# Optimization experiments

Measured on AMD Instinct MI355X. Metric: run time of the kernel, lower is better.

Reference implementation:

```python
import jax, jax.numpy as jnp
import numpy as np

EMBED = 512
NH = 8
HD = EMBED // NH
NL = 12
FFN = 2048
TD = 16  # latent_channels * patch_size**2 = 4*4


def _ln(x, g, b):
    m = x.mean(-1, keepdims=True)
    v = ((x - m) ** 2).mean(-1, keepdims=True)
    return (x - m) * jax.lax.rsqrt(v + 1e-5) * g + b


def _pos_emb(H, W, d):
    # faithful to get_2d_rope_embedding: cosine 1D embeddings along h and w, concatenated
    dh = d // 2
    inv = 1.0 / (10000.0 ** (jnp.arange(dh, dtype=jnp.float32) / dh))
    peh = jnp.cos(jnp.arange(H, dtype=jnp.float32)[:, None] * inv[None, :])  # (H, dh)
    pew = jnp.cos(jnp.arange(W, dtype=jnp.float32)[:, None] * inv[None, :])  # (W, dh)
    pe = jnp.concatenate([
        jnp.broadcast_to(peh[:, None, :], (H, W, dh)),
        jnp.broadcast_to(pew[None, :, :], (H, W, dh)),
    ], axis=-1)
    return pe.reshape(H * W, d)


def setup_inputs() -> dict:
    key = jax.random.key(0)
    ks = jax.random.split(key, 20)
    B, L = 8, 1024
    s = 0.02
    inp = {
        'x': jax.random.normal(ks[0], (B, L, TD), jnp.float32),
        'token_mask': jnp.ones((B, L), jnp.int32),
        'W_in': s * jax.random.normal(ks[1], (TD, EMBED), jnp.float32),
        'b_in': jnp.zeros((EMBED,), jnp.float32),
        'ln1_g': jnp.ones((NL, EMBED), jnp.float32),
        'ln1_b': jnp.zeros((NL, EMBED), jnp.float32),
        'Wq': s * jax.random.normal(ks[2], (NL, EMBED, EMBED), jnp.float32),
        'Wk': s * jax.random.normal(ks[3], (NL, EMBED, EMBED), jnp.float32),
        'Wv': s * jax.random.normal(ks[4], (NL, EMBED, EMBED), jnp.float32),
        'Wo': s * jax.random.normal(ks[5], (NL, EMBED, EMBED), jnp.float32),
        'ln2_g': jnp.ones((NL, EMBED), jnp.float32),
        'ln2_b': jnp.zeros((NL, EMBED), jnp.float32),
        'W1': s * jax.random.normal(ks[6], (NL, EMBED, FFN), jnp.float32),
        'W2': s * jax.random.normal(ks[7], (NL, EMBED, FFN), jnp.float32),
        'W3': s * jax.random.normal(ks[8], (NL, FFN, EMBED), jnp.float32),
        'W_out': s * jax.random.normal(ks[9], (EMBED, TD), jnp.float32),
        'b_out': jnp.zeros((TD,), jnp.float32),
        'H': 32,
        'W': 32,
    }
    return inp


def reference(x, token_mask, W_in, b_in, ln1_g, ln1_b, Wq, Wk, Wv, Wo,
              ln2_g, ln2_b, W1, W2, W3, W_out, b_out, H, W):
    B, L, _ = x.shape
    scale = 1.0 / np.sqrt(HD).astype(np.float32)
    h = x @ W_in + b_in + _pos_emb(H, W, EMBED)[None]  # (B, L, E)
    # (B,1,1,L) additive mask, -1e9 at padded positions
    mask = (token_mask == 0)[:, None, None, :].astype(h.dtype) * (-1e9)

    def block(h, p):
        g1, b1, wq, wk, wv, wo, g2, b2, w1, w2, w3 = p
        xn = _ln(h, g1, b1)
        q = (xn @ wq).reshape(B, L, NH, HD)
        k = (xn @ wk).reshape(B, L, NH, HD)
        v = (xn @ wv).reshape(B, L, NH, HD)
        s = jnp.einsum('blhd,bmhd->bhlm', q, k) * scale + mask
        a = jax.nn.softmax(s, axis=-1)
        o = jnp.einsum('bhlm,bmhd->blhd', a, v).reshape(B, L, EMBED) @ wo
        h = h + o
        xn = _ln(h, g2, b2)
        h = h + (jax.nn.silu(xn @ w1) * (xn @ w2)) @ w3
        return h, None

    h, _ = jax.lax.scan(block, h, (ln1_g, ln1_b, Wq, Wk, Wv, Wo, ln2_g, ln2_b, W1, W2, W3))
    return h @ W_out + b_out  # (B, L, TD)
```

## Files before the change

kernel.cpp:

```cpp
#include <hip/hip_runtime.h>

typedef __attribute__((ext_vector_type(8))) short short8;
typedef __attribute__((ext_vector_type(4))) float f32x4;
typedef __attribute__((ext_vector_type(4))) unsigned short us4;

#define MFMA_BF16(a,b,c) __builtin_amdgcn_mfma_f32_16x16x32_bf16((a),(b),(c),0,0,0)

__device__ __forceinline__ unsigned short f2bf(float f) {
  unsigned int u = __float_as_uint(f);
  u += 0x7fffu + ((u >> 16) & 1u);
  return (unsigned short)(u >> 16);
}

__device__ __forceinline__ int xcd_swz(int lid, int nwg) {
  return (lid & 7) * (nwg >> 3) + (lid >> 3);
}

__global__ __launch_bounds__(256) void wtrans_kernel(const float* __restrict__ src,
                                                     unsigned short* __restrict__ dst,
                                                     int R, int C) {
  __shared__ float tile[32][33];
  int c0 = blockIdx.x * 32, r0 = blockIdx.y * 32;
  const float* s = src + (size_t)blockIdx.z * R * C;
  unsigned short* d = dst + (size_t)blockIdx.z * R * C;
  int tx = threadIdx.x, ty = threadIdx.y;
#pragma unroll
  for (int i = 0; i < 32; i += 8)
    tile[ty + i][tx] = s[(size_t)(r0 + ty + i) * C + c0 + tx];
  __syncthreads();
#pragma unroll
  for (int i = 0; i < 32; i += 8)
    d[(size_t)(c0 + ty + i) * R + r0 + tx] = f2bf(tile[tx][ty + i]);
}

__global__ __launch_bounds__(128) void embed_kernel(const float* __restrict__ x,
                                                    const float* __restrict__ Win,
                                                    const float* __restrict__ bin,
                                                    float* __restrict__ h) {
  __shared__ float xs[16];
  int m = blockIdx.x, t = threadIdx.x;
  if (t < 16) xs[t] = x[m * 16 + t];
  __syncthreads();
  int l = m & 1023, hi = l >> 5, wi = l & 31;
#pragma unroll
  for (int e0 = 0; e0 < 512; e0 += 128) {
    int e = e0 + t;
    float a = bin[e];
#pragma unroll
    for (int kk = 0; kk < 16; kk++) a += xs[kk] * Win[kk * 512 + e];
    int j = e & 255;
    float p = (e < 256) ? (float)hi : (float)wi;
    float inv = expf((float)j * (-9.210340371976184f / 256.0f));
    a += cosf(p * inv);
    h[(size_t)m * 512 + e] = a;
  }
}

__global__ __launch_bounds__(256) void ln_kernel(const float* __restrict__ h,
                                                 const float* __restrict__ gw,
                                                 const float* __restrict__ bw,
                                                 unsigned short* __restrict__ xn) {
  int row = blockIdx.x * 4 + (threadIdx.x >> 6);
  int lane = threadIdx.x & 63;
  const f32x4* hr = (const f32x4*)&h[(size_t)row * 512];
  f32x4 v0 = hr[lane], v1 = hr[lane + 64];
  float s = v0[0]+v0[1]+v0[2]+v0[3] + v1[0]+v1[1]+v1[2]+v1[3];
  float q = v0[0]*v0[0]+v0[1]*v0[1]+v0[2]*v0[2]+v0[3]*v0[3]
          + v1[0]*v1[0]+v1[1]*v1[1]+v1[2]*v1[2]+v1[3]*v1[3];
#pragma unroll
  for (int o = 1; o < 64; o <<= 1) { s += __shfl_xor(s, o); q += __shfl_xor(q, o); }
  float mean = s * (1.0f / 512.0f);
  float var = q * (1.0f / 512.0f) - mean * mean;
  float rstd = rsqrtf(var + 1e-5f);
  f32x4 g0 = ((const f32x4*)gw)[lane], g1 = ((const f32x4*)gw)[lane + 64];
  f32x4 b0 = ((const f32x4*)bw)[lane], b1 = ((const f32x4*)bw)[lane + 64];
  us4 w0, w1;
#pragma unroll
  for (int r = 0; r < 4; r++) {
    w0[r] = f2bf((v0[r] - mean) * rstd * g0[r] + b0[r]);
    w1[r] = f2bf((v1[r] - mean) * rstd * g1[r] + b1[r]);
  }
  *(us4*)&xn[(size_t)row * 512 + lane * 4] = w0;
  *(us4*)&xn[(size_t)row * 512 + 256 + lane * 4] = w1;
}

__global__ __launch_bounds__(256) void qkv_gemm(const unsigned short* __restrict__ xn,
                                                const unsigned short* __restrict__ wtq,
                                                const unsigned short* __restrict__ wtk,
                                                const unsigned short* __restrict__ wtv,
                                                unsigned short* __restrict__ qo,
                                                unsigned short* __restrict__ ko,
                                                unsigned short* __restrict__ vt) {
  __shared__ short8 As[1024];
  __shared__ short8 Bs[1024];
  int n0 = blockIdx.x * 128, m0 = blockIdx.y * 128;
  int sel = n0 >> 9;
  const short8* wt = (const short8*)(sel == 0 ? wtq : sel == 1 ? wtk : wtv);
  int nw = n0 & 511;
  const short8* A8 = (const short8*)xn;
  int tid = threadIdx.x, wid = tid >> 6, lane = tid & 63;
  int wr = wid >> 1, wc = wid & 1, c16 = lane & 15, g = lane >> 4;
  const short8* aSrc[4];
  const short8* bSrc[4];
#pragma unroll
  for (int s = 0; s < 4; s++) {
    int sub = wid * 4 + s, rg = sub >> 1, kc = sub & 1;
    aSrc[s] = A8 + (size_t)(m0 + rg * 16 + c16) * 64 + kc * 4 + g;
    bSrc[s] = wt + (size_t)(nw + rg * 16 + c16) * 64 + kc * 4 + g;
  }
  f32x4 acc[4][4] = {};
  short8 ra[4], rb[4];
#pragma unroll
  for (int s = 0; s < 4; s++) { ra[s] = aSrc[s][0]; rb[s] = bSrc[s][0]; }
  for (int kt = 0; kt < 8; kt++) {
    __syncthreads();
#pragma unroll
    for (int s = 0; s < 4; s++) {
      As[(wid * 4 + s) * 64 + lane] = ra[s];
      Bs[(wid * 4 + s) * 64 + lane] = rb[s];
    }
    if (kt < 7) {
#pragma unroll
      for (int s = 0; s < 4; s++) {
        ra[s] = aSrc[s][(kt + 1) * 8];
        rb[s] = bSrc[s][(kt + 1) * 8];
      }
    }
    __syncthreads();
#pragma unroll
    for (int kc = 0; kc < 2; kc++) {
      short8 af[4], bf[4];
#pragma unroll
      for (int mf = 0; mf < 4; mf++) af[mf] = As[((wr * 4 + mf) * 2 + kc) * 64 + lane];
#pragma unroll
      for (int nf = 0; nf < 4; nf++) bf[nf] = Bs[((wc * 4 + nf) * 2 + kc) * 64 + lane];
#pragma unroll
      for (int mf = 0; mf < 4; mf++)
#pragma unroll
        for (int nf = 0; nf < 4; nf++)
          acc[mf][nf] = MFMA_BF16(af[mf], bf[nf], acc[mf][nf]);
    }
  }
  if (sel < 2) {
    unsigned short* out = sel == 0 ? qo : ko;
#pragma unroll
    for (int mf = 0; mf < 4; mf++)
#pragma unroll
      for (int nf = 0; nf < 4; nf++) {
        int col = nw + wc * 64 + nf * 16 + c16;
#pragma unroll
        for (int r = 0; r < 4; r++) {
          int row = m0 + wr * 64 + mf * 16 + g * 4 + r;
          out[(size_t)row * 512 + col] = f2bf(acc[mf][nf][r]);
        }
      }
  } else {
    int b8 = (m0 >> 10) * 8;
    int loff = (m0 & 1023) + wr * 64;
#pragma unroll
    for (int mf = 0; mf < 4; mf++)
#pragma unroll
      for (int nf = 0; nf < 4; nf++) {
        int c = nw + wc * 64 + nf * 16 + c16;
        int bh = b8 + (c >> 6), d = c & 63;
        us4 w;
#pragma unroll
        for (int r = 0; r < 4; r++) w[r] = f2bf(acc[mf][nf][r]);
        *(us4*)&vt[(size_t)(bh * 64 + d) * 1024 + loff + mf * 16 + g * 4] = w;
      }
  }
}

__global__ __launch_bounds__(256) void gemm_res(const unsigned short* __restrict__ A,
                                                const unsigned short* __restrict__ Wt,
                                                float* __restrict__ h, int Kd8, int nkt64) {
  __shared__ short8 As[1024];
  __shared__ short8 Bs[1024];
  int n0 = blockIdx.x * 128, m0 = blockIdx.y * 128;
  const short8* A8 = (const short8*)A;
  const short8* W8 = (const short8*)Wt;
  int tid = threadIdx.x, wid = tid >> 6, lane = tid & 63;
  int wr = wid >> 1, wc = wid & 1, c16 = lane & 15, g = lane >> 4;
  const short8* aSrc[4];
  const short8* bSrc[4];
#pragma unroll
  for (int s = 0; s < 4; s++) {
    int sub = wid * 4 + s, rg = sub >> 1, kc = sub & 1;
    aSrc[s] = A8 + (size_t)(m0 + rg * 16 + c16) * Kd8 + kc * 4 + g;
    bSrc[s] = W8 + (size_t)(n0 + rg * 16 + c16) * Kd8 + kc * 4 + g;
  }
  f32x4 acc[4][4] = {};
  short8 ra[4], rb[4];
#pragma unroll
  for (int s = 0; s < 4; s++) { ra[s] = aSrc[s][0]; rb[s] = bSrc[s][0]; }
  for (int kt = 0; kt < nkt64; kt++) {
    __syncthreads();
#pragma unroll
    for (int s = 0; s < 4; s++) {
      As[(wid * 4 + s) * 64 + lane] = ra[s];
      Bs[(wid * 4 + s) * 64 + lane] = rb[s];
    }
    if (kt + 1 < nkt64) {
#pragma unroll
      for (int s = 0; s < 4; s++) {
        ra[s] = aSrc[s][(kt + 1) * 8];
        rb[s] = bSrc[s][(kt + 1) * 8];
      }
    }
    __syncthreads();
#pragma unroll
    for (int kc = 0; kc < 2; kc++) {
      short8 af[4], bf[4];
#pragma unroll
      for (int mf = 0; mf < 4; mf++) af[mf] = As[((wr * 4 + mf) * 2 + kc) * 64 + lane];
#pragma unroll
      for (int nf = 0; nf < 4; nf++) bf[nf] = Bs[((wc * 4 + nf) * 2 + kc) * 64 + lane];
#pragma unroll
      for (int mf = 0; mf < 4; mf++)
#pragma unroll
        for (int nf = 0; nf < 4; nf++)
          acc[mf][nf] = MFMA_BF16(af[mf], bf[nf], acc[mf][nf]);
    }
  }
#pragma unroll
  for (int mf = 0; mf < 4; mf++)
#pragma unroll
    for (int nf = 0; nf < 4; nf++) {
      int col = n0 + wc * 64 + nf * 16 + c16;
#pragma unroll
      for (int r = 0; r < 4; r++) {
        int row = m0 + wr * 64 + mf * 16 + g * 4 + r;
        h[(size_t)row * 512 + col] += acc[mf][nf][r];
      }
    }
}

__global__ __launch_bounds__(256) void ffn_gemm(const unsigned short* __restrict__ xn,
                                                const unsigned short* __restrict__ w1t,
                                                const unsigned short* __restrict__ w2t,
                                                unsigned short* __restrict__ gout) {
  __shared__ short8 As[1024];
  __shared__ short8 B1s[1024];
  __shared__ short8 B2s[1024];
  int n0 = blockIdx.x * 128, m0 = blockIdx.y * 128;
  const short8* A8 = (const short8*)xn;
  const short8* W18 = (const short8*)w1t;
  const short8* W28 = (const short8*)w2t;
  int tid = threadIdx.x, wid = tid >> 6, lane = tid & 63;
  int wr = wid >> 1, wc = wid & 1, c16 = lane & 15, g = lane >> 4;
  const short8* aSrc[4];
  const short8* b1Src[4];
  const short8* b2Src[4];
#pragma unroll
  for (int s = 0; s < 4; s++) {
    int sub = wid * 4 + s, rg = sub >> 1, kc = sub & 1;
    aSrc[s]  = A8  + (size_t)(m0 + rg * 16 + c16) * 64 + kc * 4 + g;
    b1Src[s] = W18 + (size_t)(n0 + rg * 16 + c16) * 64 + kc * 4 + g;
    b2Src[s] = W28 + (size_t)(n0 + rg * 16 + c16) * 64 + kc * 4 + g;
  }
  f32x4 acc1[4][4] = {};
  f32x4 acc2[4][4] = {};
  short8 ra[4], rb1[4], rb2[4];
#pragma unroll
  for (int s = 0; s < 4; s++) {
    ra[s] = aSrc[s][0]; rb1[s] = b1Src[s][0]; rb2[s] = b2Src[s][0];
  }
  for (int kt = 0; kt < 8; kt++) {
    __syncthreads();
#pragma unroll
    for (int s = 0; s < 4; s++) {
      As [(wid * 4 + s) * 64 + lane] = ra[s];
      B1s[(wid * 4 + s) * 64 + lane] = rb1[s];
      B2s[(wid * 4 + s) * 64 + lane] = rb2[s];
    }
    if (kt < 7) {
#pragma unroll
      for (int s = 0; s < 4; s++) {
        ra[s]  = aSrc[s][(kt + 1) * 8];
        rb1[s] = b1Src[s][(kt + 1) * 8];
        rb2[s] = b2Src[s][(kt + 1) * 8];
      }
    }
    __syncthreads();
#pragma unroll
    for (int kc = 0; kc < 2; kc++) {
      short8 af[4], b1f[4], b2f[4];
#pragma unroll
      for (int mf = 0; mf < 4; mf++) af[mf] = As[((wr * 4 + mf) * 2 + kc) * 64 + lane];
#pragma unroll
      for (int nf = 0; nf < 4; nf++) {
        b1f[nf] = B1s[((wc * 4 + nf) * 2 + kc) * 64 + lane];
        b2f[nf] = B2s[((wc * 4 + nf) * 2 + kc) * 64 + lane];
      }
#pragma unroll
      for (int mf = 0; mf < 4; mf++)
#pragma unroll
        for (int nf = 0; nf < 4; nf++) {
          acc1[mf][nf] = MFMA_BF16(af[mf], b1f[nf], acc1[mf][nf]);
          acc2[mf][nf] = MFMA_BF16(af[mf], b2f[nf], acc2[mf][nf]);
        }
    }
  }
#pragma unroll
  for (int mf = 0; mf < 4; mf++)
#pragma unroll
    for (int nf = 0; nf < 4; nf++) {
      int col = n0 + wc * 64 + nf * 16 + c16;
#pragma unroll
      for (int r = 0; r < 4; r++) {
        int row = m0 + wr * 64 + mf * 16 + g * 4 + r;
        float xx = acc1[mf][nf][r];
        float yy = acc2[mf][nf][r];
        float sg = xx / (1.0f + __expf(-xx));
        gout[(size_t)row * 2048 + col] = f2bf(sg * yy);
      }
    }
}

__global__ __launch_bounds__(256) void attn_kernel(const unsigned short* __restrict__ q,
                                                   const unsigned short* __restrict__ k,
                                                   const unsigned short* __restrict__ vt,
                                                   const int* __restrict__ tmsk,
                                                   unsigned short* __restrict__ o) {
  __shared__ short8 Ks[512];
  __shared__ short8 Vs[512];
  __shared__ uint2  Pb[2048];
  __shared__ f32x4  maskv[256];

  int s = xcd_swz((int)blockIdx.x, 512);
  int qb = s & 7;
  int bh = s >> 3;
  int b = bh >> 3, hh = bh & 7;
  int tid = threadIdx.x, wid = tid >> 6, lane = tid & 63;
  int c16 = lane & 15, gq = lane >> 4;
  int qrow0 = qb * 128 + wid * 32;

  const short8* q8 = (const short8*)q;
  const short8* k8 = (const short8*)k;
  const short8* v8 = (const short8*)vt;

  short8 qf[2][2];
#pragma unroll
  for (int nf = 0; nf < 2; nf++)
#pragma unroll
    for (int dc = 0; dc < 2; dc++)
      qf[nf][dc] = q8[(size_t)(b * 1024 + qrow0 + nf * 16 + c16) * 64 + hh * 8 + dc * 4 + gq];

  {
    int4 mm = ((const int4*)(tmsk + b * 1024))[tid];
    f32x4 ma;
    ma[0] = (mm.x == 0) ? -1e9f : 0.0f;
    ma[1] = (mm.y == 0) ? -1e9f : 0.0f;
    ma[2] = (mm.z == 0) ? -1e9f : 0.0f;
    ma[3] = (mm.w == 0) ? -1e9f : 0.0f;
    maskv[tid] = ma;
  }

  short8 rk[2], rv[2];
#pragma unroll
  for (int ss = 0; ss < 2; ss++) {
    int sub = wid * 2 + ss;
    rk[ss] = k8[(size_t)(b * 1024 + (sub >> 1) * 16 + c16) * 64 + hh * 8 + (sub & 1) * 4 + gq];
    rv[ss] = v8[(size_t)(bh * 64 + (sub >> 1) * 16 + c16) * 128 + (sub & 1) * 4 + gq];
  }

  float mrun[2] = {-1e30f, -1e30f};
  float lrun[2] = {0.0f, 0.0f};
  f32x4 accO[4][2] = {};

  for (int kt = 0; kt < 16; kt++) {
    __syncthreads();
#pragma unroll
    for (int ss = 0; ss < 2; ss++) {
      int sub = wid * 2 + ss;
      Ks[sub * 64 + lane] = rk[ss];
      Vs[sub * 64 + lane] = rv[ss];
    }
    if (kt < 15) {
      int kt2 = kt + 1;
#pragma unroll
      for (int ss = 0; ss < 2; ss++) {
        int sub = wid * 2 + ss;
        rk[ss] = k8[(size_t)(b * 1024 + kt2 * 64 + (sub >> 1) * 16 + c16) * 64 + hh * 8 + (sub & 1) * 4 + gq];
        rv[ss] = v8[(size_t)(bh * 64 + (sub >> 1) * 16 + c16) * 128 + kt2 * 8 + (sub & 1) * 4 + gq];
      }
    }
    __syncthreads();

    f32x4 sT[4][2] = {};
#pragma unroll
    for (int mf = 0; mf < 4; mf++) {
      short8 ka0 = Ks[(mf * 2 + 0) * 64 + lane];
      short8 ka1 = Ks[(mf * 2 + 1) * 64 + lane];
#pragma unroll
      for (int nf = 0; nf < 2; nf++) {
        sT[mf][nf] = MFMA_BF16(ka0, qf[nf][0], sT[mf][nf]);
        sT[mf][nf] = MFMA_BF16(ka1, qf[nf][1], sT[mf][nf]);
      }
    }

#pragma unroll
    for (int nf = 0; nf < 2; nf++) {
      float pv[4][4];
      float tm = -1e30f;
#pragma unroll
      for (int mf = 0; mf < 4; mf++) {
        f32x4 mk = maskv[kt * 16 + mf * 4 + gq];
#pragma unroll
        for (int r = 0; r < 4; r++) {
          float sv = sT[mf][nf][r] * 0.125f + mk[r];
          pv[mf][r] = sv;
          tm = fmaxf(tm, sv);
        }
      }
      tm = fmaxf(tm, __shfl_xor(tm, 16));
      tm = fmaxf(tm, __shfl_xor(tm, 32));
      float mn = fmaxf(mrun[nf], tm);
      float fac = __expf(mrun[nf] - mn);
      mrun[nf] = mn;
      float ts = 0.0f;
#pragma unroll
      for (int mf = 0; mf < 4; mf++)
#pragma unroll
        for (int r = 0; r < 4; r++) {
          float p = __expf(pv[mf][r] - mn);
          pv[mf][r] = p;
          ts += p;
        }
      ts += __shfl_xor(ts, 16);
      ts += __shfl_xor(ts, 32);
      lrun[nf] = lrun[nf] * fac + ts;
#pragma unroll
      for (int dmf = 0; dmf < 4; dmf++) accO[dmf][nf] *= fac;
#pragma unroll
      for (int mf = 0; mf < 4; mf++) {
        unsigned lo = (unsigned)f2bf(pv[mf][0]) | ((unsigned)f2bf(pv[mf][1]) << 16);
        unsigned hi = (unsigned)f2bf(pv[mf][2]) | ((unsigned)f2bf(pv[mf][3]) << 16);
        int kk = mf >> 1;
        int gr = (mf & 1) * 2 + (gq >> 1);
        uint2 t2; t2.x = lo; t2.y = hi;
        Pb[wid * 512 + ((nf * 2 + kk) * 64 + gr * 16 + c16) * 2 + (gq & 1)] = t2;
      }
    }
    __syncthreads();

    const short8* Pb8 = (const short8*)Pb;
#pragma unroll
    for (int nf = 0; nf < 2; nf++) {
      short8 pb0 = Pb8[wid * 256 + (nf * 2 + 0) * 64 + lane];
      short8 pb1 = Pb8[wid * 256 + (nf * 2 + 1) * 64 + lane];
#pragma unroll
      for (int dmf = 0; dmf < 4; dmf++) {
        short8 va0 = Vs[(dmf * 2 + 0) * 64 + lane];
        short8 va1 = Vs[(dmf * 2 + 1) * 64 + lane];
        accO[dmf][nf] = MFMA_BF16(va0, pb0, accO[dmf][nf]);
        accO[dmf][nf] = MFMA_BF16(va1, pb1, accO[dmf][nf]);
      }
    }
  }

#pragma unroll
  for (int nf = 0; nf < 2; nf++) {
    float inv = 1.0f / lrun[nf];
    int row = b * 1024 + qrow0 + nf * 16 + c16;
#pragma unroll
    for (int dmf = 0; dmf < 4; dmf++) {
      us4 w;
#pragma unroll
      for (int r = 0; r < 4; r++) w[r] = f2bf(accO[dmf][nf][r] * inv);
      *(us4*)&o[(size_t)row * 512 + hh * 64 + dmf * 16 + gq * 4] = w;
    }
  }
}

__global__ __launch_bounds__(128) void out_kernel(const float* __restrict__ h,
                                                  const float* __restrict__ Wout,
                                                  const float* __restrict__ bout,
                                                  float* __restrict__ out) {
  __shared__ f32x4 hs4[8][128];
  __shared__ f32x4 Ws4[16][129];
  int t = threadIdx.x;
  int rb = blockIdx.x * 8;
  float* hsf = (float*)hs4;
  float* wsf = (float*)Ws4;
  for (int i = t; i < 4096; i += 128) hsf[i] = h[(size_t)rb * 512 + i];
  for (int i = t; i < 8192; i += 128) wsf[(i & 15) * 516 + (i >> 4)] = Wout[i];
  __syncthreads();
  int r = t >> 4, c = t & 15;
  float acc = bout[c];
  for (int k4 = 0; k4 < 128; k4++) {
    f32x4 a = hs4[r][k4];
    f32x4 w = Ws4[c][k4];
    acc += a[0]*w[0] + a[1]*w[1] + a[2]*w[2] + a[3]*w[3];
  }
  out[(rb + r) * 16 + c] = acc;
}

extern "C" void kernel_launch(void* const* d_in, const int* in_sizes, int n_in,
                              void* d_out, int out_size, void* d_ws, size_t ws_size,
                              hipStream_t stream) {
  const float* x    = (const float*)d_in[0];
  const int*   tmsk = (const int*)d_in[1];
  const float* Win  = (const float*)d_in[2];
  const float* bin  = (const float*)d_in[3];
  const float* ln1g = (const float*)d_in[4];
  const float* ln1b = (const float*)d_in[5];
  const float* Wq   = (const float*)d_in[6];
  const float* Wk   = (const float*)d_in[7];
  const float* Wv   = (const float*)d_in[8];
  const float* Wo   = (const float*)d_in[9];
  const float* ln2g = (const float*)d_in[10];
  const float* ln2b = (const float*)d_in[11];
  const float* W1   = (const float*)d_in[12];
  const float* W2   = (const float*)d_in[13];
  const float* W3   = (const float*)d_in[14];
  const float* Wout = (const float*)d_in[15];
  const float* bout = (const float*)d_in[16];
  float* outp = (float*)d_out;

  char* ws = (char*)d_ws;
  unsigned short* wtq = (unsigned short*)(ws + 0);
  unsigned short* wtk = (unsigned short*)(ws + 6291456);
  unsigned short* wtv = (unsigned short*)(ws + 12582912);
  unsigned short* wto = (unsigned short*)(ws + 18874368);
  unsigned short* wt1 = (unsigned short*)(ws + 25165824);
  unsigned short* wt2 = (unsigned short*)(ws + 50331648);
  unsigned short* wt3 = (unsigned short*)(ws + 75497472);
  float*          h   = (float*)(ws + 100663296);
  unsigned short* xn  = (unsigned short*)(ws + 117440512);
  unsigned short* qb  = (unsigned short*)(ws + 125829120);
  unsigned short* kb  = (unsigned short*)(ws + 134217728);
  unsigned short* vtb = (unsigned short*)(ws + 150994944);
  unsigned short* ob  = (unsigned short*)(ws + 159383552);
  unsigned short* gb  = (unsigned short*)(ws + 167772160);

  dim3 tb(32, 8);
  wtrans_kernel<<<dim3(16, 16, 12), tb, 0, stream>>>(Wq, wtq, 512, 512);
  wtrans_kernel<<<dim3(16, 16, 12), tb, 0, stream>>>(Wk, wtk, 512, 512);
  wtrans_kernel<<<dim3(16, 16, 12), tb, 0, stream>>>(Wv, wtv, 512, 512);
  wtrans_kernel<<<dim3(16, 16, 12), tb, 0, stream>>>(Wo, wto, 512, 512);
  wtrans_kernel<<<dim3(64, 16, 12), tb, 0, stream>>>(W1, wt1, 512, 2048);
  wtrans_kernel<<<dim3(64, 16, 12), tb, 0, stream>>>(W2, wt2, 512, 2048);
  wtrans_kernel<<<dim3(16, 64, 12), tb, 0, stream>>>(W3, wt3, 2048, 512);

  embed_kernel<<<8192, 128, 0, stream>>>(x, Win, bin, h);

  for (int l = 0; l < 12; l++) {
    ln_kernel<<<2048, 256, 0, stream>>>(h, ln1g + l * 512, ln1b + l * 512, xn);
    qkv_gemm<<<dim3(12, 64), 256, 0, stream>>>(xn,
        wtq + (size_t)l * 262144, wtk + (size_t)l * 262144, wtv + (size_t)l * 262144,
        qb, kb, vtb);
    attn_kernel<<<512, 256, 0, stream>>>(qb, kb, vtb, tmsk, ob);
    gemm_res<<<dim3(4, 64), 256, 0, stream>>>(ob, wto + (size_t)l * 262144, h, 64, 8);
    ln_kernel<<<2048, 256, 0, stream>>>(h, ln2g + l * 512, ln2b + l * 512, xn);
    ffn_gemm<<<dim3(16, 64), 256, 0, stream>>>(xn,
        wt1 + (size_t)l * 1048576, wt2 + (size_t)l * 1048576, gb);
    gemm_res<<<dim3(4, 64), 256, 0, stream>>>(gb, wt3 + (size_t)l * 1048576, h, 256, 32);
  }
  out_kernel<<<1024, 128, 0, stream>>>(h, Wout, bout, outp);

  (void)in_sizes; (void)n_in; (void)out_size; (void)ws_size;
}
```

Baseline: 2.519 ms.

## Enlarge QKV/FFN GEMM tiles to 256 rows and add lazy softmax rescaling

The QKV and FFN GEMMs now use 512-thread blocks covering 256 rows by 128 columns, so each weight tile loaded into shared memory is reused by twice as many rows and the grid shrinks by half. The attention softmax moves to base-2 exponentials with the log2(e) factor folded into the score scale and mask. It also skips rescaling the running max and accumulators unless some lane's max grows by more than 8. The goal is less weight traffic and fewer exp and rescale operations, at the cost of more LDS per block, possibly lower occupancy, and a looser running-max bound in the softmax.

```diff
diff --git a/kernel.cpp b/kernel.cpp
--- a/kernel.cpp
+++ b/kernel.cpp
@@ -84,16 +84,16 @@
   *(us4*)&xn[(size_t)row * 512 + 256 + lane * 4] = w1;
 }
 
-__global__ __launch_bounds__(256) void qkv_gemm(const unsigned short* __restrict__ xn,
+__global__ __launch_bounds__(512) void qkv_gemm(const unsigned short* __restrict__ xn,
                                                 const unsigned short* __restrict__ wtq,
                                                 const unsigned short* __restrict__ wtk,
                                                 const unsigned short* __restrict__ wtv,
                                                 unsigned short* __restrict__ qo,
                                                 unsigned short* __restrict__ ko,
                                                 unsigned short* __restrict__ vt) {
-  __shared__ short8 As[1024];
+  __shared__ short8 As[2048];
   __shared__ short8 Bs[1024];
-  int n0 = blockIdx.x * 128, m0 = blockIdx.y * 128;
+  int n0 = blockIdx.x * 128, m0 = blockIdx.y * 256;
   int sel = n0 >> 9;
   const short8* wt = (const short8*)(sel == 0 ? wtq : sel == 1 ? wtk : wtv);
   int nw = n0 & 511;
@@ -101,30 +101,34 @@
   int tid = threadIdx.x, wid = tid >> 6, lane = tid & 63;
   int wr = wid >> 1, wc = wid & 1, c16 = lane & 15, g = lane >> 4;
   const short8* aSrc[4];
-  const short8* bSrc[4];
+  const short8* bSrc[2];
 #pragma unroll
   for (int s = 0; s < 4; s++) {
     int sub = wid * 4 + s, rg = sub >> 1, kc = sub & 1;
     aSrc[s] = A8 + (size_t)(m0 + rg * 16 + c16) * 64 + kc * 4 + g;
+  }
+#pragma unroll
+  for (int s = 0; s < 2; s++) {
+    int sub = wid * 2 + s, rg = sub >> 1, kc = sub & 1;
     bSrc[s] = wt + (size_t)(nw + rg * 16 + c16) * 64 + kc * 4 + g;
   }
   f32x4 acc[4][4] = {};
-  short8 ra[4], rb[4];
-#pragma unroll
-  for (int s = 0; s < 4; s++) { ra[s] = aSrc[s][0]; rb[s] = bSrc[s][0]; }
+  short8 ra[4], rb[2];
+#pragma unroll
+  for (int s = 0; s < 4; s++) ra[s] = aSrc[s][0];
+#pragma unroll
+  for (int s = 0; s < 2; s++) rb[s] = bSrc[s][0];
   for (int kt = 0; kt < 8; kt++) {
     __syncthreads();
 #pragma unroll
-    for (int s = 0; s < 4; s++) {
-      As[(wid * 4 + s) * 64 + lane] = ra[s];
-      Bs[(wid * 4 + s) * 64 + lane] = rb[s];
-    }
+    for (int s = 0; s < 4; s++) As[(wid * 4 + s) * 64 + lane] = ra[s];
+#pragma unroll
+    for (int s = 0; s < 2; s++) Bs[(wid * 2 + s) * 64 + lane] = rb[s];
     if (kt < 7) {
 #pragma unroll
-      for (int s = 0; s < 4; s++) {
-        ra[s] = aSrc[s][(kt + 1) * 8];
-        rb[s] = bSrc[s][(kt + 1) * 8];
-      }
+      for (int s = 0; s < 4; s++) ra[s] = aSrc[s][(kt + 1) * 8];
+#pragma unroll
+      for (int s = 0; s < 2; s++) rb[s] = bSrc[s][(kt + 1) * 8];
     }
     __syncthreads();
 #pragma unroll
@@ -235,48 +239,54 @@
     }
 }
 
-__global__ __launch_bounds__(256) void ffn_gemm(const unsigned short* __restrict__ xn,
+__global__ __launch_bounds__(512) void ffn_gemm(const unsigned short* __restrict__ xn,
                                                 const unsigned short* __restrict__ w1t,
                                                 const unsigned short* __restrict__ w2t,
                                                 unsigned short* __restrict__ gout) {
-  __shared__ short8 As[1024];
+  __shared__ short8 As[2048];
   __shared__ short8 B1s[1024];
   __shared__ short8 B2s[1024];
-  int n0 = blockIdx.x * 128, m0 = blockIdx.y * 128;
+  int n0 = blockIdx.x * 128, m0 = blockIdx.y * 256;
   const short8* A8 = (const short8*)xn;
   const short8* W18 = (const short8*)w1t;
   const short8* W28 = (const short8*)w2t;
   int tid = threadIdx.x, wid = tid >> 6, lane = tid & 63;
   int wr = wid >> 1, wc = wid & 1, c16 = lane & 15, g = lane >> 4;
   const short8* aSrc[4];
-  const short8* b1Src[4];
-  const short8* b2Src[4];
+  const short8* b1Src[2];
+  const short8* b2Src[2];
 #pragma unroll
   for (int s = 0; s < 4; s++) {
     int sub = wid * 4 + s, rg = sub >> 1, kc = sub & 1;
-    aSrc[s]  = A8  + (size_t)(m0 + rg * 16 + c16) * 64 + kc * 4 + g;
+    aSrc[s] = A8 + (size_t)(m0 + rg * 16 + c16) * 64 + kc * 4 + g;
+  }
+#pragma unroll
+  for (int s = 0; s < 2; s++) {
+    int sub = wid * 2 + s, rg = sub >> 1, kc = sub & 1;
     b1Src[s] = W18 + (size_t)(n0 + rg * 16 + c16) * 64 + kc * 4 + g;
     b2Src[s] = W28 + (size_t)(n0 + rg * 16 + c16) * 64 + kc * 4 + g;
   }
   f32x4 acc1[4][4] = {};
   f32x4 acc2[4][4] = {};
-  short8 ra[4], rb1[4], rb2[4];
-#pragma unroll
-  for (int s = 0; s < 4; s++) {
-    ra[s] = aSrc[s][0]; rb1[s] = b1Src[s][0]; rb2[s] = b2Src[s][0];
-  }
+  short8 ra[4], rb1[2], rb2[2];
+#pragma unroll
+  for (int s = 0; s < 4; s++) ra[s] = aSrc[s][0];
+#pragma unroll
+  for (int s = 0; s < 2; s++) { rb1[s] = b1Src[s][0]; rb2[s] = b2Src[s][0]; }
   for (int kt = 0; kt < 8; kt++) {
     __syncthreads();
 #pragma unroll
-    for (int s = 0; s < 4; s++) {
-      As [(wid * 4 + s) * 64 + lane] = ra[s];
-      B1s[(wid * 4 + s) * 64 + lane] = rb1[s];
-      B2s[(wid * 4 + s) * 64 + lane] = rb2[s];
+    for (int s = 0; s < 4; s++) As[(wid * 4 + s) * 64 + lane] = ra[s];
+#pragma unroll
+    for (int s = 0; s < 2; s++) {
+      B1s[(wid * 2 + s) * 64 + lane] = rb1[s];
+      B2s[(wid * 2 + s) * 64 + lane] = rb2[s];
     }
     if (kt < 7) {
 #pragma unroll
-      for (int s = 0; s < 4; s++) {
-        ra[s]  = aSrc[s][(kt + 1) * 8];
+      for (int s = 0; s < 4; s++) ra[s] = aSrc[s][(kt + 1) * 8];
+#pragma unroll
+      for (int s = 0; s < 2; s++) {
         rb1[s] = b1Src[s][(kt + 1) * 8];
         rb2[s] = b2Src[s][(kt + 1) * 8];
       }
@@ -349,10 +359,10 @@
   {
     int4 mm = ((const int4*)(tmsk + b * 1024))[tid];
     f32x4 ma;
-    ma[0] = (mm.x == 0) ? -1e9f : 0.0f;
-    ma[1] = (mm.y == 0) ? -1e9f : 0.0f;
-    ma[2] = (mm.z == 0) ? -1e9f : 0.0f;
-    ma[3] = (mm.w == 0) ? -1e9f : 0.0f;
+    ma[0] = (mm.x == 0) ? -1.442695e9f : 0.0f;
+    ma[1] = (mm.y == 0) ? -1.442695e9f : 0.0f;
+    ma[2] = (mm.z == 0) ? -1.442695e9f : 0.0f;
+    ma[3] = (mm.w == 0) ? -1.442695e9f : 0.0f;
     maskv[tid] = ma;
   }
 
@@ -367,6 +377,7 @@
   float mrun[2] = {-1e30f, -1e30f};
   float lrun[2] = {0.0f, 0.0f};
   f32x4 accO[4][2] = {};
+  const float SCL = 0.125f * 1.4426950408889634f;
 
   for (int kt = 0; kt < 16; kt++) {
     __syncthreads();
@@ -408,30 +419,33 @@
         f32x4 mk = maskv[kt * 16 + mf * 4 + gq];
 #pragma unroll
         for (int r = 0; r < 4; r++) {
-          float sv = sT[mf][nf][r] * 0.125f + mk[r];
+          float sv = sT[mf][nf][r] * SCL + mk[r];
           pv[mf][r] = sv;
           tm = fmaxf(tm, sv);
         }
       }
       tm = fmaxf(tm, __shfl_xor(tm, 16));
       tm = fmaxf(tm, __shfl_xor(tm, 32));
-      float mn = fmaxf(mrun[nf], tm);
-      float fac = __expf(mrun[nf] - mn);
-      mrun[nf] = mn;
+      if (!__all(tm - mrun[nf] <= 8.0f)) {
+        float mn = fmaxf(mrun[nf], tm);
+        float fac = exp2f(mrun[nf] - mn);
+        mrun[nf] = mn;
+        lrun[nf] *= fac;
+#pragma unroll
+        for (int dmf = 0; dmf < 4; dmf++) accO[dmf][nf] *= fac;
+      }
       float ts = 0.0f;
 #pragma unroll
       for (int mf = 0; mf < 4; mf++)
 #pragma unroll
         for (int r = 0; r < 4; r++) {
-          float p = __expf(pv[mf][r] - mn);
+          float p = exp2f(pv[mf][r] - mrun[nf]);
           pv[mf][r] = p;
           ts += p;
         }
       ts += __shfl_xor(ts, 16);
       ts += __shfl_xor(ts, 32);
-      lrun[nf] = lrun[nf] * fac + ts;
-#pragma unroll
-      for (int dmf = 0; dmf < 4; dmf++) accO[dmf][nf] *= fac;
+      lrun[nf] += ts;
 #pragma unroll
       for (int mf = 0; mf < 4; mf++) {
         unsigned lo = (unsigned)f2bf(pv[mf][0]) | ((unsigned)f2bf(pv[mf][1]) << 16);
@@ -547,13 +561,13 @@
 
   for (int l = 0; l < 12; l++) {
     ln_kernel<<<2048, 256, 0, stream>>>(h, ln1g + l * 512, ln1b + l * 512, xn);
-    qkv_gemm<<<dim3(12, 64), 256, 0, stream>>>(xn,
+    qkv_gemm<<<dim3(12, 32), 512, 0, stream>>>(xn,
         wtq + (size_t)l * 262144, wtk + (size_t)l * 262144, wtv + (size_t)l * 262144,
         qb, kb, vtb);
     attn_kernel<<<512, 256, 0, stream>>>(qb, kb, vtb, tmsk, ob);
     gemm_res<<<dim3(4, 64), 256, 0, stream>>>(ob, wto + (size_t)l * 262144, h, 64, 8);
     ln_kernel<<<2048, 256, 0, stream>>>(h, ln2g + l * 512, ln2b + l * 512, xn);
-    ffn_gemm<<<dim3(16, 64), 256, 0, stream>>>(xn,
+    ffn_gemm<<<dim3(16, 32), 512, 0, stream>>>(xn,
         wt1 + (size_t)l * 1048576, wt2 + (size_t)l * 1048576, gb);
     gemm_res<<<dim3(4, 64), 256, 0, stream>>>(gb, wt3 + (size_t)l * 1048576, h, 256, 32);
   }
```

Result: faster. 2.309 ms (-8.3%).
